# Kernel optimization log

Measured on AMD Instinct MI355X. Metric: run time of the kernel, lower is better.

## Reference

```python
import jax, jax.numpy as jnp
import numpy as np

B, H, W, C = 2, 64, 64, 96
DIN, NST, RNK, K = 192, 16, 6, 4
L = H * W


def _make_ids():
    idx = np.arange(L).reshape(H, W)
    p0 = idx.reshape(-1)
    p1 = idx.T.reshape(-1)
    p2 = p0[::-1].copy()
    p3 = p1[::-1].copy()
    scan = np.stack([p0, p1, p2, p3]).astype(np.int32)
    inv = np.stack([np.argsort(p) for p in scan]).astype(np.int32)
    return jnp.asarray(scan), jnp.asarray(inv)


def setup_inputs() -> dict:
    key = jax.random.key(0)
    ks = jax.random.split(key, 10)
    scan_ids, inv_ids = _make_ids()
    std = RNK ** -0.5
    # dt bias init: inverse-softplus of dt ~ LogUniform(1e-3, 1e-1), as in VMM.dt_init
    u = jax.random.uniform(ks[5], (K, DIN))
    dt = jnp.exp(u * (np.log(0.1) - np.log(0.001)) + np.log(0.001))
    dt_b = dt + jnp.log(-jnp.expm1(-dt))
    return {
        "x": jax.random.normal(ks[0], (B, H, W, C), jnp.float32),
        "W_in": jax.random.normal(ks[1], (2 * DIN, C), jnp.float32) * 0.02,
        "conv_w": jax.random.normal(ks[2], (DIN, 1, 3, 3), jnp.float32) * 0.1,
        "conv_b": jnp.zeros((DIN,), jnp.float32),
        "x_proj_w": jax.random.normal(ks[3], (K, RNK + 2 * NST, DIN), jnp.float32) * 0.02,
        "dt_w": jax.random.uniform(ks[4], (K, DIN, RNK), jnp.float32, -std, std),
        "dt_b": dt_b.astype(jnp.float32),
        "A_logs": jnp.log(jnp.tile(jnp.arange(1, NST + 1, dtype=jnp.float32)[None], (K * DIN, 1))),
        "Ds": jnp.ones((K * DIN,), jnp.float32),
        "gate_w": jax.random.normal(ks[6], (4 * DIN, 4), jnp.float32) * 0.1,  # grouped 1x1 conv, groups=DIN
        "gate_b": jnp.zeros((4 * DIN,), jnp.float32),
        "ln_g": jnp.ones((DIN,), jnp.float32),
        "ln_b": jnp.zeros((DIN,), jnp.float32),
        "W_out": jax.random.normal(ks[7], (C, DIN), jnp.float32) * 0.02,
        "scan_ids": scan_ids,
        "inv_ids": inv_ids,
    }


def _forward(x, W_in, conv_w, conv_b, x_proj_w, dt_w, dt_b, A_logs, Ds, gate_w, gate_b, ln_g, ln_b, W_out, scan_ids, inv_ids):
    b, h, w, c = x.shape
    l = h * w
    din = conv_w.shape[0]
    k = x_proj_w.shape[0]
    nst = A_logs.shape[1]
    rnk = dt_w.shape[2]
    # in_proj + split into x / gate z
    xz = x @ W_in.T
    xc, z = jnp.split(xz, 2, axis=-1)
    xc = jnp.transpose(xc, (0, 3, 1, 2))  # (b, din, h, w)
    # depthwise 3x3 conv + SiLU
    xc = jax.lax.conv_general_dilated(
        xc, conv_w, (1, 1), "SAME", feature_group_count=din,
        dimension_numbers=("NCHW", "OIHW", "NCHW")) + conv_b[None, :, None, None]
    xc = jax.nn.silu(xc)
    # multi-directional gather (mair_ids_scan)
    xf = xc.reshape(b, din, l)
    xs = jnp.moveaxis(xf[:, :, scan_ids], 2, 1)  # (b, k, din, l)
    # x_proj (grouped 1x1 conv) -> dt, B, C
    x_dbl = jnp.einsum("bkdl,krd->bkrl", xs, x_proj_w)
    dts, Bs, Cs = jnp.split(x_dbl, [rnk, rnk + nst], axis=2)  # (b,k,rnk,l),(b,k,n,l),(b,k,n,l)
    delta = jax.nn.softplus(jnp.einsum("bkrl,kdr->bkdl", dts, dt_w) + dt_b[None, :, :, None])
    A = -jnp.exp(A_logs).reshape(k, din, nst)
    dA = jnp.exp(delta[..., None] * A[None, :, :, None, :])              # (b,k,d,l,n)
    dBu = (delta * xs)[..., None] * jnp.moveaxis(Bs, 2, 3)[:, :, None]   # (b,k,d,l,n)

    def step(hst, inp):
        da, dbu = inp
        hst = da * hst + dbu
        return hst, hst

    h0 = jnp.zeros((b, k, din, nst), jnp.float32)
    _, hs = jax.lax.scan(step, h0, (jnp.moveaxis(dA, 3, 0), jnp.moveaxis(dBu, 3, 0)))  # (l,b,k,d,n)
    ys = jnp.einsum("lbkdn,bknl->bkdl", hs, Cs) + xs * Ds.reshape(k, din)[None, :, :, None]
    # inverse scatter (mair_ids_inverse) + concat along channels
    y = jax.vmap(lambda yk, ik: yk[..., ik], in_axes=(1, 0), out_axes=1)(ys, inv_ids)
    y = y.reshape(b, k * din, h, w)
    # ShuffleAttn gating: group = din, group_channels = k
    shuf = y.reshape(b, k, din, h, w).transpose(0, 2, 1, 3, 4).reshape(b, k * din, h, w)
    pooled = shuf.mean(axis=(2, 3)).reshape(b, din, k)
    gate = jax.nn.sigmoid(jnp.einsum("bgi,goi->bgo", pooled, gate_w.reshape(din, k, k)) + gate_b.reshape(din, k))
    gate = gate.transpose(0, 2, 1).reshape(b, k * din)  # channel_rearrange
    y = y * gate[:, :, None, None]
    # sum the 4 direction branches
    y = y.reshape(b, k, din, h, w).sum(axis=1)
    y = jnp.transpose(y, (0, 2, 3, 1))  # (b,h,w,din)
    # LayerNorm(d_inner)
    mu = y.mean(-1, keepdims=True)
    var = ((y - mu) ** 2).mean(-1, keepdims=True)
    y = (y - mu) / jnp.sqrt(var + 1e-5) * ln_g + ln_b
    y = y * jax.nn.silu(z)
    return y @ W_out.T


def reference(x, W_in, conv_w, conv_b, x_proj_w, dt_w, dt_b, A_logs, Ds, gate_w, gate_b, ln_g, ln_b, W_out, scan_ids, inv_ids):
    return _forward(x, W_in, conv_w, conv_b, x_proj_w, dt_w, dt_b, A_logs, Ds, gate_w, gate_b, ln_g, ln_b, W_out, scan_ids, inv_ids)
```

## Files before the change

kernel.cpp:

```cpp
#include <hip/hip_runtime.h>
#include <math.h>

#define BB 2
#define CC 96
#define DIN 192
#define NST 16
#define RNK 6
#define KK 4
#define LL 4096
#define RTOT (RNK + 2*NST)


__global__ __launch_bounds__(256) void k_inproj(const float* __restrict__ x,
        const float* __restrict__ W_in, float* __restrict__ xc_pre,
        float* __restrict__ z_silu) {
    __shared__ float lx[96*65];
    __shared__ float wt[48*196];
    int b = blockIdx.y, z = blockIdx.z;
    int l0 = blockIdx.x * 64;
    int t = threadIdx.x;
    for (int i = 0; i < 24; ++i) {
        int e = t + 256*i;
        int l = e / 96, c = e % 96;
        lx[c*65 + l] = x[((size_t)(b*LL + l0 + l))*96 + c];
    }
    int lg = t & 15;
    int og = t >> 4;
    float acc[4][12];
    #pragma unroll
    for (int j = 0; j < 4; ++j)
        #pragma unroll
        for (int q = 0; q < 12; ++q) acc[j][q] = 0.f;
    for (int p = 0; p < 2; ++p) {
        __syncthreads();
        for (int i = 0; i < 36; ++i) {
            int e = t + 256*i;
            int cc = e % 48, oc = e / 48;
            wt[cc*196 + oc] = W_in[((size_t)(z*192 + oc))*96 + p*48 + cc];
        }
        __syncthreads();
        #pragma unroll 2
        for (int cc = 0; cc < 48; ++cc) {
            int c = p*48 + cc;
            float x0 = lx[c*65 + 4*lg + 0];
            float x1 = lx[c*65 + 4*lg + 1];
            float x2 = lx[c*65 + 4*lg + 2];
            float x3 = lx[c*65 + 4*lg + 3];
            const float* wr = &wt[cc*196 + 12*og];
            float4 w0 = *(const float4*)(wr);
            float4 w1 = *(const float4*)(wr + 4);
            float4 w2 = *(const float4*)(wr + 8);
            float wv[12] = {w0.x,w0.y,w0.z,w0.w, w1.x,w1.y,w1.z,w1.w,
                            w2.x,w2.y,w2.z,w2.w};
            #pragma unroll
            for (int q = 0; q < 12; ++q) {
                acc[0][q] += x0*wv[q];
                acc[1][q] += x1*wv[q];
                acc[2][q] += x2*wv[q];
                acc[3][q] += x3*wv[q];
            }
        }
    }
    float* dst = (z == 0) ? xc_pre : z_silu;
    #pragma unroll
    for (int j = 0; j < 4; ++j) {
        int l = l0 + 4*lg + j;
        size_t base = (size_t)(b*LL + l)*DIN + 12*og;
        #pragma unroll
        for (int q = 0; q < 12; ++q) {
            float v = acc[j][q];
            if (z) v = v / (1.f + __expf(-v));
            dst[base + q] = v;
        }
    }
}

__global__ __launch_bounds__(256) void k_conv(const float* __restrict__ xc,
        const float* __restrict__ cw, const float* __restrict__ cb,
        float* __restrict__ out) {
    int gid = blockIdx.x*256 + threadIdx.x;
    int d = gid % DIN;
    int r = gid / DIN;
    int l = r & 4095, b = r >> 12;
    int w = l & 63, h = l >> 6;
    float acc = cb[d];
    #pragma unroll
    for (int dh = -1; dh <= 1; ++dh) {
        int h2 = h + dh;
        bool okh = (h2 >= 0) && (h2 < 64);
        #pragma unroll
        for (int dw = -1; dw <= 1; ++dw) {
            int w2 = w + dw;
            if (okh && w2 >= 0 && w2 < 64)
                acc += xc[((size_t)(b*LL + h2*64 + w2))*DIN + d] * cw[d*9 + (dh+1)*3 + (dw+1)];
        }
    }
    out[((size_t)(b*LL + l))*DIN + d] = acc / (1.f + __expf(-acc));
}

__global__ __launch_bounds__(512) void k_proj(const float* __restrict__ xconv,
        const int* __restrict__ scan_ids, const float* __restrict__ xpw,
        float* __restrict__ dts, float* __restrict__ Bs, float* __restrict__ Cs) {
    __shared__ float lxs[96*65];
    __shared__ float lw[RTOT*96];
    __shared__ float lbc[64*33];
    __shared__ int lsid[64];
    int k = blockIdx.y, b = blockIdx.z;
    int l0 = blockIdx.x * 64;
    int t = threadIdx.x;
    if (t < 64) lsid[t] = scan_ids[k*LL + l0 + t];
    int l = t & 63;
    int rg = __builtin_amdgcn_readfirstlane(t >> 6);
    float acc[5];
    #pragma unroll
    for (int j = 0; j < 5; ++j) acc[j] = 0.f;
    for (int p = 0; p < 2; ++p) {
        __syncthreads();
        for (int i = 0; i < 12; ++i) {
            int e = t + 512*i;
            int dd = e % 96, ll = e / 96;
            lxs[dd*65 + ll] = xconv[((size_t)(b*LL + lsid[ll]))*DIN + p*96 + dd];
        }
        for (int i = 0; i < 8; ++i) {
            int e = t + 512*i;
            if (e < RTOT*96) {
                int r = e / 96, dd = e % 96;
                lw[r*96 + dd] = xpw[(size_t)k*RTOT*DIN + r*DIN + p*96 + dd];
            }
        }
        __syncthreads();
        for (int dd = 0; dd < 96; dd += 4) {
            float x0 = lxs[(dd+0)*65 + l];
            float x1 = lxs[(dd+1)*65 + l];
            float x2 = lxs[(dd+2)*65 + l];
            float x3 = lxs[(dd+3)*65 + l];
            #pragma unroll
            for (int j = 0; j < 5; ++j) {
                int r = rg + 8*j;
                if (r < RTOT) {
                    float4 w = *(const float4*)&lw[r*96 + dd];
                    acc[j] += x0*w.x + x1*w.y + x2*w.z + x3*w.w;
                }
            }
        }
    }
    int bk = b*KK + k;
    #pragma unroll
    for (int j = 0; j < 5; ++j) {
        int r = rg + 8*j;
        if (r < RNK)       dts[((size_t)bk*LL + l0 + l)*8 + r] = acc[j];
        else if (r < RTOT) lbc[l*33 + (r - RNK)] = acc[j];
    }
    __syncthreads();
    size_t rowb = ((size_t)bk*LL + l0)*NST;
    for (int i = 0; i < 2; ++i) {
        int e = t + 512*i;
        int n = e & 15, ll = e >> 4;
        Bs[rowb + ll*NST + n] = lbc[ll*33 + n];
        Cs[rowb + ll*NST + n] = lbc[ll*33 + 16 + n];
    }
}

__global__ __launch_bounds__(384) void k_scan1(const float* __restrict__ xconv,
        const float* __restrict__ Bs, const float* __restrict__ Cs,
        const float* __restrict__ dts, const float* __restrict__ dtw,
        const float* __restrict__ dtb,
        const int* __restrict__ scan_ids, const float* __restrict__ A_logs,
        const float* __restrict__ Ds,
        float* __restrict__ y_dirs, float* __restrict__ segA,
        float* __restrict__ segB, int SL) {
    int seg = blockIdx.x, bk = blockIdx.y;
    int b = bk >> 2, k = bk & 3;
    int t = threadIdx.x;
    int half = t & 1, d = t >> 1;
    int l0 = seg * SL;
    float Av[8];
    {
        const float4* ap = (const float4*)(A_logs + ((k*DIN + d)*NST + half*8));
        float4 a0 = ap[0], a1 = ap[1];
        Av[0]=-__expf(a0.x); Av[1]=-__expf(a0.y); Av[2]=-__expf(a0.z); Av[3]=-__expf(a0.w);
        Av[4]=-__expf(a1.x); Av[5]=-__expf(a1.y); Av[6]=-__expf(a1.z); Av[7]=-__expf(a1.w);
    }
    float Dv = Ds[k*DIN + d];
    float wdt[RNK];
    float bdt = dtb[k*DIN + d];
    #pragma unroll
    for (int r = 0; r < RNK; ++r) wdt[r] = dtw[(k*DIN + d)*RNK + r];
    float h[8];
    #pragma unroll
    for (int n = 0; n < 8; ++n) h[n] = 0.f;
    float sumdv = 0.f;
    const int* sid = scan_ids + k*LL + l0;
    int ln = sid[0];
    float xn = xconv[((size_t)(b*LL + ln))*DIN + d];
    for (int li = 0; li < SL; ++li) {
        int l = ln;
        float xv = xn;
        if (li + 1 < SL) {
            ln = sid[li + 1];
            xn = xconv[((size_t)(b*LL + ln))*DIN + d];
        }
        const float* dr = dts + ((size_t)bk*LL + l0 + li)*8;
        float aa = bdt;
        #pragma unroll
        for (int r = 0; r < RNK; ++r) aa += dr[r]*wdt[r];
        float dv = fmaxf(aa, 0.f) + __logf(1.f + __expf(-fabsf(aa)));
        sumdv += dv;
        float dxv = dv * xv;
        const float* br = Bs + ((size_t)bk*LL + l0 + li)*NST + half*8;
        const float* cr = Cs + ((size_t)bk*LL + l0 + li)*NST + half*8;
        float4 b0 = *(const float4*)br;
        float4 b1 = *(const float4*)(br + 4);
        float4 c0v = *(const float4*)cr;
        float4 c1v = *(const float4*)(cr + 4);
        float bb[8] = {b0.x,b0.y,b0.z,b0.w, b1.x,b1.y,b1.z,b1.w};
        float cc[8] = {c0v.x,c0v.y,c0v.z,c0v.w, c1v.x,c1v.y,c1v.z,c1v.w};
        float y = 0.f;
        #pragma unroll
        for (int n = 0; n < 8; ++n) {
            float e2 = __expf(dv * Av[n]);
            h[n] = e2*h[n] + dxv*bb[n];
            y += h[n]*cc[n];
        }
        y += __shfl_xor(y, 1);
        if (half == 0) {
            y += xv * Dv;
            y_dirs[((size_t)(bk*LL + l))*DIN + d] = y;
        }
    }
    float a[8];
    #pragma unroll
    for (int n = 0; n < 8; ++n) a[n] = __expf(Av[n]*sumdv);
    size_t base = (((size_t)bk*gridDim.x + seg)*DIN + d)*NST + half*8;
    *(float4*)&segA[base]     = make_float4(a[0],a[1],a[2],a[3]);
    *(float4*)&segA[base + 4] = make_float4(a[4],a[5],a[6],a[7]);
    *(float4*)&segB[base]     = make_float4(h[0],h[1],h[2],h[3]);
    *(float4*)&segB[base + 4] = make_float4(h[4],h[5],h[6],h[7]);
}

__global__ __launch_bounds__(256) void k_scan2(const float* segA,
        const float* segB, float* hinit, int SEGC) {
    int idx = blockIdx.x*256 + threadIdx.x;
    if (idx >= BB*KK*DIN*NST) return;
    int bk = idx / (DIN*NST);
    int dn = idx % (DIN*NST);
    const size_t stride = DIN*NST;
    size_t o = (size_t)bk*SEGC*stride + dn;
    float h = 0.f;
    for (int s = 0; s < SEGC; s += 8) {
        float av[8], bv[8];
        #pragma unroll
        for (int j = 0; j < 8; ++j) {
            av[j] = segA[o + j*stride];
            bv[j] = segB[o + j*stride];
        }
        #pragma unroll
        for (int j = 0; j < 8; ++j) {
            hinit[o + j*stride] = h;
            h = av[j]*h + bv[j];
        }
        o += 8*stride;
    }
}

__global__ __launch_bounds__(384) void k_apply(const float* __restrict__ Cs,
        const float* __restrict__ dts, const float* __restrict__ dtw,
        const float* __restrict__ dtb,
        const int* __restrict__ scan_ids, const float* __restrict__ A_logs,
        const float* __restrict__ hinit,
        float* __restrict__ y_dirs, float* __restrict__ poolsum, int SL) {
    int seg = blockIdx.x, bk = blockIdx.y;
    int b = bk >> 2, k = bk & 3;
    int t = threadIdx.x;
    int half = t & 1, d = t >> 1;
    int l0 = seg * SL;
    float Av[8];
    {
        const float4* ap = (const float4*)(A_logs + ((k*DIN + d)*NST + half*8));
        float4 a0 = ap[0], a1 = ap[1];
        Av[0]=-__expf(a0.x); Av[1]=-__expf(a0.y); Av[2]=-__expf(a0.z); Av[3]=-__expf(a0.w);
        Av[4]=-__expf(a1.x); Av[5]=-__expf(a1.y); Av[6]=-__expf(a1.z); Av[7]=-__expf(a1.w);
    }
    float Av0 = -__expf(A_logs[(k*DIN + d)*NST]);
    bool okl = true;
    #pragma unroll
    for (int q = 0; q < 8; ++q) {
        float m = (float)(half*8 + q + 1);
        okl = okl && (fabsf(Av[q] - m*Av0) <= 1e-4f*m);
    }
    int fast = __all(okl);
    float h0[8];
    {
        size_t base = (((size_t)bk*gridDim.x + seg)*DIN + d)*NST + half*8;
        float4 v0 = *(const float4*)&hinit[base];
        float4 v1 = *(const float4*)&hinit[base + 4];
        h0[0]=v0.x; h0[1]=v0.y; h0[2]=v0.z; h0[3]=v0.w;
        h0[4]=v1.x; h0[5]=v1.y; h0[6]=v1.z; h0[7]=v1.w;
    }
    float wdt[RNK];
    float bdt = dtb[k*DIN + d];
    #pragma unroll
    for (int r = 0; r < RNK; ++r) wdt[r] = dtw[(k*DIN + d)*RNK + r];
    float cum = 0.f;
    float pool = 0.f;
    const int* sid = scan_ids + k*LL + l0;
    for (int li = 0; li < SL; ++li) {
        int l = sid[li];
        const float* dr = dts + ((size_t)bk*LL + l0 + li)*8;
        float aa = bdt;
        #pragma unroll
        for (int r = 0; r < RNK; ++r) aa += dr[r]*wdt[r];
        cum += fmaxf(aa, 0.f) + __logf(1.f + __expf(-fabsf(aa)));
        const float* cr = Cs + ((size_t)bk*LL + l0 + li)*NST + half*8;
        float4 c0v = *(const float4*)cr;
        float4 c1v = *(const float4*)(cr + 4);
        float cc[8] = {c0v.x,c0v.y,c0v.z,c0v.w, c1v.x,c1v.y,c1v.z,c1v.w};
        float g;
        if (fast) {
            float E = __expf(Av0 * cum);
            g = 0.f;
            #pragma unroll
            for (int q = 7; q >= 0; --q) g = g*E + cc[q]*h0[q];
            g *= E;
            if (half) {
                float E2 = E*E, E4 = E2*E2;
                g *= E4*E4;
            }
        } else {
            g = 0.f;
            #pragma unroll
            for (int q = 0; q < 8; ++q)
                g += cc[q]*h0[q]*__expf(Av[q]*cum);
        }
        g += __shfl_xor(g, 1);
        if (half == 0) {
            size_t yo = ((size_t)(bk*LL + l))*DIN + d;
            float y = y_dirs[yo] + g;
            y_dirs[yo] = y;
            pool += y;
        }
    }
    if (half == 0) atomicAdd(&poolsum[(b*DIN + d)*KK + k], pool);
}

__global__ __launch_bounds__(256) void k_final(const float* __restrict__ y_dirs,
        const float* __restrict__ poolsum, const float* __restrict__ gw,
        const float* __restrict__ gb, const float* __restrict__ z_silu,
        const float* __restrict__ lng, const float* __restrict__ lnb,
        const float* __restrict__ Wout, float* __restrict__ out) {
    __shared__ float buf[16*193];
    __shared__ float lgate[DIN*KK];
    __shared__ float lmu[16], lrs[16];
    int b = blockIdx.y;
    int l0 = blockIdx.x * 16;
    int t = threadIdx.x;
    for (int e = t; e < DIN*KK; e += 256) {
        int d = e >> 2, o = e & 3;
        float acc = gb[d*KK + o];
        #pragma unroll
        for (int i = 0; i < KK; ++i)
            acc += (poolsum[(b*DIN + d)*KK + i] * (1.f/LL)) * gw[(d*KK + o)*KK + i];
        lgate[d*KK + o] = 1.f/(1.f + __expf(-acc));
    }
    __syncthreads();
    for (int i = 0; i < 12; ++i) {
        int e = t + 256*i;
        int d = e % DIN, l = e / DIN;
        float acc = 0.f;
        #pragma unroll
        for (int k = 0; k < KK; ++k)
            acc += y_dirs[((size_t)((b*KK + k)*LL + l0 + l))*DIN + d] * lgate[d*KK + k];
        buf[l*193 + d] = acc;
    }
    __syncthreads();
    int l2 = t >> 4, q = t & 15;
    float s = 0.f, s2 = 0.f;
    for (int i = 0; i < 12; ++i) {
        float v = buf[l2*193 + q + 16*i];
        s += v; s2 += v*v;
    }
    s += __shfl_xor(s, 1);  s2 += __shfl_xor(s2, 1);
    s += __shfl_xor(s, 2);  s2 += __shfl_xor(s2, 2);
    s += __shfl_xor(s, 4);  s2 += __shfl_xor(s2, 4);
    s += __shfl_xor(s, 8);  s2 += __shfl_xor(s2, 8);
    if (q == 0) {
        float mu = s * (1.f/DIN);
        float var = s2 * (1.f/DIN) - mu*mu;
        lmu[l2] = mu;
        lrs[l2] = rsqrtf(var + 1e-5f);
    }
    __syncthreads();
    for (int i = 0; i < 12; ++i) {
        int e = t + 256*i;
        int d = e % DIN, l = e / DIN;
        float v = buf[l*193 + d];
        float tv = (v - lmu[l]) * lrs[l] * lng[d] + lnb[d];
        tv *= z_silu[((size_t)(b*LL + l0 + l))*DIN + d];
        buf[l*193 + d] = tv;
    }
    __syncthreads();
    int l = t & 15;
    int c0 = (t >> 4) * 6;
    float acc[6];
    #pragma unroll
    for (int cc = 0; cc < 6; ++cc) acc[cc] = 0.f;
    for (int d = 0; d < DIN; ++d) {
        float v = buf[l*193 + d];
        #pragma unroll
        for (int cc = 0; cc < 6; ++cc)
            acc[cc] += v * Wout[(c0 + cc)*DIN + d];
    }
    #pragma unroll
    for (int cc = 0; cc < 6; ++cc)
        out[((size_t)(b*LL + l0 + l))*CC + c0 + cc] = acc[cc];
}

extern "C" void kernel_launch(void* const* d_in, const int* in_sizes, int n_in,
                              void* d_out, int out_size, void* d_ws, size_t ws_size,
                              hipStream_t stream) {
    const float* x      = (const float*)d_in[0];
    const float* W_in   = (const float*)d_in[1];
    const float* conv_w = (const float*)d_in[2];
    const float* conv_b = (const float*)d_in[3];
    const float* xpw    = (const float*)d_in[4];
    const float* dt_w   = (const float*)d_in[5];
    const float* dt_b   = (const float*)d_in[6];
    const float* A_logs = (const float*)d_in[7];
    const float* Ds     = (const float*)d_in[8];
    const float* gate_w = (const float*)d_in[9];
    const float* gate_b = (const float*)d_in[10];
    const float* ln_g   = (const float*)d_in[11];
    const float* ln_b   = (const float*)d_in[12];
    const float* W_out  = (const float*)d_in[13];
    const int* scan_ids = (const int*)d_in[14];
    float* out = (float*)d_out;

    const size_t baseF = 6291456ull + 2ull*1572864 + 262144ull + 2ull*524288 + 3072;
    int SEGC = 16;
    if ((baseF + 2ull*128*24576)*4 <= ws_size) SEGC = 128;
    else if ((baseF + 2ull*64*24576)*4 <= ws_size) SEGC = 64;
    else if ((baseF + 2ull*32*24576)*4 <= ws_size) SEGC = 32;
    int SL = LL / SEGC;
    size_t segF = (size_t)SEGC * 24576;

    float* ws      = (float*)d_ws;
    float* y_dirs  = ws;
    float* xc_pre  = ws;
    float* z_silu  = y_dirs  + 6291456;
    float* xconv   = z_silu  + 1572864;
    float* dts     = xconv   + 1572864;
    float* Bs      = dts     + 262144;
    float* Cs      = Bs      + 524288;
    float* poolsum = Cs      + 524288;
    float* segA    = poolsum + 3072;
    float* segB    = segA    + segF;
    float* hinit   = segA;

    hipMemsetAsync(poolsum, 0, 1536*sizeof(float), stream);

    k_inproj<<<dim3(LL/64, BB, 2), 256, 0, stream>>>(x, W_in, xc_pre, z_silu);
    k_conv<<<(BB*DIN*LL)/256, 256, 0, stream>>>(xc_pre, conv_w, conv_b, xconv);
    k_proj<<<dim3(LL/64, KK, BB), 512, 0, stream>>>(xconv, scan_ids, xpw,
                                                    dts, Bs, Cs);
    k_scan1<<<dim3(SEGC, BB*KK), 384, 0, stream>>>(xconv, Bs, Cs, dts, dt_w, dt_b,
                                                   scan_ids, A_logs, Ds,
                                                   y_dirs, segA, segB, SL);
    k_scan2<<<(BB*KK*DIN*NST + 255)/256, 256, 0, stream>>>(segA, segB, hinit, SEGC);
    k_apply<<<dim3(SEGC, BB*KK), 384, 0, stream>>>(Cs, dts, dt_w, dt_b,
                                                   scan_ids, A_logs, hinit,
                                                   y_dirs, poolsum, SL);
    k_final<<<dim3(LL/16, BB), 256, 0, stream>>>(y_dirs, poolsum, gate_w, gate_b,
                                                 z_silu, ln_g, ln_b, W_out, out);
}
```

Before: 280.4 us.

## Vectorize global loads and stores with float4 and prefetch scan operands

Several kernels switch to float4 global loads and stores: the in-projection staging and output, the depthwise conv (each thread now handles 4 channels with weights in registers), the gathers in the x-projection, and the gating, LayerNorm and out-projection stages of the final kernel. The in-projection now loops over both halves (x and gate) inside one block, so the input tile is loaded once, at the price of half as many blocks. The scan and apply loops software-prefetch the next step's dt, B and C values into registers to hide load latency on the serial recurrence. The final buffer's row stride is padded to 196 so rows stay 16-byte aligned for float4 access.

```diff
diff --git a/kernel.cpp b/kernel.cpp
--- a/kernel.cpp
+++ b/kernel.cpp
@@ -16,61 +16,74 @@
         float* __restrict__ z_silu) {
     __shared__ float lx[96*65];
     __shared__ float wt[48*196];
-    int b = blockIdx.y, z = blockIdx.z;
+    int b = blockIdx.y;
     int l0 = blockIdx.x * 64;
     int t = threadIdx.x;
-    for (int i = 0; i < 24; ++i) {
-        int e = t + 256*i;
-        int l = e / 96, c = e % 96;
-        lx[c*65 + l] = x[((size_t)(b*LL + l0 + l))*96 + c];
+    for (int i = 0; i < 6; ++i) {
+        int e4 = t + 256*i;
+        int c4 = e4 % 24, l = e4 / 24;
+        float4 v = *(const float4*)&x[((size_t)(b*LL + l0 + l))*96 + 4*c4];
+        lx[(4*c4+0)*65 + l] = v.x;
+        lx[(4*c4+1)*65 + l] = v.y;
+        lx[(4*c4+2)*65 + l] = v.z;
+        lx[(4*c4+3)*65 + l] = v.w;
     }
     int lg = t & 15;
     int og = t >> 4;
-    float acc[4][12];
-    #pragma unroll
-    for (int j = 0; j < 4; ++j)
-        #pragma unroll
-        for (int q = 0; q < 12; ++q) acc[j][q] = 0.f;
-    for (int p = 0; p < 2; ++p) {
-        __syncthreads();
-        for (int i = 0; i < 36; ++i) {
-            int e = t + 256*i;
-            int cc = e % 48, oc = e / 48;
-            wt[cc*196 + oc] = W_in[((size_t)(z*192 + oc))*96 + p*48 + cc];
-        }
-        __syncthreads();
-        #pragma unroll 2
-        for (int cc = 0; cc < 48; ++cc) {
-            int c = p*48 + cc;
-            float x0 = lx[c*65 + 4*lg + 0];
-            float x1 = lx[c*65 + 4*lg + 1];
-            float x2 = lx[c*65 + 4*lg + 2];
-            float x3 = lx[c*65 + 4*lg + 3];
-            const float* wr = &wt[cc*196 + 12*og];
-            float4 w0 = *(const float4*)(wr);
-            float4 w1 = *(const float4*)(wr + 4);
-            float4 w2 = *(const float4*)(wr + 8);
-            float wv[12] = {w0.x,w0.y,w0.z,w0.w, w1.x,w1.y,w1.z,w1.w,
-                            w2.x,w2.y,w2.z,w2.w};
+    for (int z = 0; z < 2; ++z) {
+        float acc[4][12];
+        #pragma unroll
+        for (int j = 0; j < 4; ++j)
+            #pragma unroll
+            for (int q = 0; q < 12; ++q) acc[j][q] = 0.f;
+        for (int p = 0; p < 2; ++p) {
+            __syncthreads();
+            for (int i = 0; i < 9; ++i) {
+                int e4 = t + 256*i;
+                int cc4 = e4 % 12, oc = e4 / 12;
+                float4 v = *(const float4*)&W_in[((size_t)(z*192 + oc))*96 + p*48 + 4*cc4];
+                wt[(4*cc4+0)*196 + oc] = v.x;
+                wt[(4*cc4+1)*196 + oc] = v.y;
+                wt[(4*cc4+2)*196 + oc] = v.z;
+                wt[(4*cc4+3)*196 + oc] = v.w;
+            }
+            __syncthreads();
+            #pragma unroll 2
+            for (int cc = 0; cc < 48; ++cc) {
+                int c = p*48 + cc;
+                float x0 = lx[c*65 + 4*lg + 0];
+                float x1 = lx[c*65 + 4*lg + 1];
+                float x2 = lx[c*65 + 4*lg + 2];
+                float x3 = lx[c*65 + 4*lg + 3];
+                const float* wr = &wt[cc*196 + 12*og];
+                float4 w0 = *(const float4*)(wr);
+                float4 w1 = *(const float4*)(wr + 4);
+                float4 w2 = *(const float4*)(wr + 8);
+                float wv[12] = {w0.x,w0.y,w0.z,w0.w, w1.x,w1.y,w1.z,w1.w,
+                                w2.x,w2.y,w2.z,w2.w};
+                #pragma unroll
+                for (int q = 0; q < 12; ++q) {
+                    acc[0][q] += x0*wv[q];
+                    acc[1][q] += x1*wv[q];
+                    acc[2][q] += x2*wv[q];
+                    acc[3][q] += x3*wv[q];
+                }
+            }
+        }
+        float* dst = (z == 0) ? xc_pre : z_silu;
+        #pragma unroll
+        for (int j = 0; j < 4; ++j) {
+            int l = l0 + 4*lg + j;
+            size_t base = (size_t)(b*LL + l)*DIN + 12*og;
+            float v[12];
             #pragma unroll
             for (int q = 0; q < 12; ++q) {
-                acc[0][q] += x0*wv[q];
-                acc[1][q] += x1*wv[q];
-                acc[2][q] += x2*wv[q];
-                acc[3][q] += x3*wv[q];
-            }
-        }
-    }
-    float* dst = (z == 0) ? xc_pre : z_silu;
-    #pragma unroll
-    for (int j = 0; j < 4; ++j) {
-        int l = l0 + 4*lg + j;
-        size_t base = (size_t)(b*LL + l)*DIN + 12*og;
-        #pragma unroll
-        for (int q = 0; q < 12; ++q) {
-            float v = acc[j][q];
-            if (z) v = v / (1.f + __expf(-v));
-            dst[base + q] = v;
+                float a = acc[j][q];
+                v[q] = z ? a/(1.f + __expf(-a)) : a;
+            }
+            *(float4*)&dst[base]     = make_float4(v[0],v[1],v[2],v[3]);
+            *(float4*)&dst[base + 4] = make_float4(v[4],v[5],v[6],v[7]);
+            *(float4*)&dst[base + 8] = make_float4(v[8],v[9],v[10],v[11]);
         }
     }
 }
@@ -79,11 +92,17 @@
         const float* __restrict__ cw, const float* __restrict__ cb,
         float* __restrict__ out) {
     int gid = blockIdx.x*256 + threadIdx.x;
-    int d = gid % DIN;
-    int r = gid / DIN;
+    int dq = gid % 48;
+    int r = gid / 48;
     int l = r & 4095, b = r >> 12;
     int w = l & 63, h = l >> 6;
-    float acc = cb[d];
+    int d0 = dq*4;
+    float4 acc = *(const float4*)&cb[d0];
+    float wreg[4][9];
+    #pragma unroll
+    for (int j = 0; j < 4; ++j)
+        #pragma unroll
+        for (int tp = 0; tp < 9; ++tp) wreg[j][tp] = cw[(d0+j)*9 + tp];
     #pragma unroll
     for (int dh = -1; dh <= 1; ++dh) {
         int h2 = h + dh;
@@ -91,11 +110,22 @@
         #pragma unroll
         for (int dw = -1; dw <= 1; ++dw) {
             int w2 = w + dw;
-            if (okh && w2 >= 0 && w2 < 64)
-                acc += xc[((size_t)(b*LL + h2*64 + w2))*DIN + d] * cw[d*9 + (dh+1)*3 + (dw+1)];
-        }
-    }
-    out[((size_t)(b*LL + l))*DIN + d] = acc / (1.f + __expf(-acc));
+            if (okh && w2 >= 0 && w2 < 64) {
+                float4 v = *(const float4*)&xc[((size_t)(b*LL + h2*64 + w2))*DIN + d0];
+                int tp = (dh+1)*3 + (dw+1);
+                acc.x += v.x*wreg[0][tp];
+                acc.y += v.y*wreg[1][tp];
+                acc.z += v.z*wreg[2][tp];
+                acc.w += v.w*wreg[3][tp];
+            }
+        }
+    }
+    float4 o;
+    o.x = acc.x/(1.f + __expf(-acc.x));
+    o.y = acc.y/(1.f + __expf(-acc.y));
+    o.z = acc.z/(1.f + __expf(-acc.z));
+    o.w = acc.w/(1.f + __expf(-acc.w));
+    *(float4*)&out[((size_t)(b*LL + l))*DIN + d0] = o;
 }
 
 __global__ __launch_bounds__(512) void k_proj(const float* __restrict__ xconv,
@@ -116,16 +146,21 @@
     for (int j = 0; j < 5; ++j) acc[j] = 0.f;
     for (int p = 0; p < 2; ++p) {
         __syncthreads();
-        for (int i = 0; i < 12; ++i) {
-            int e = t + 512*i;
-            int dd = e % 96, ll = e / 96;
-            lxs[dd*65 + ll] = xconv[((size_t)(b*LL + lsid[ll]))*DIN + p*96 + dd];
-        }
-        for (int i = 0; i < 8; ++i) {
-            int e = t + 512*i;
-            if (e < RTOT*96) {
-                int r = e / 96, dd = e % 96;
-                lw[r*96 + dd] = xpw[(size_t)k*RTOT*DIN + r*DIN + p*96 + dd];
+        for (int i = 0; i < 3; ++i) {
+            int e4 = t + 512*i;
+            int dd4 = e4 % 24, ll = e4 / 24;
+            float4 v = *(const float4*)&xconv[((size_t)(b*LL + lsid[ll]))*DIN + p*96 + 4*dd4];
+            lxs[(4*dd4+0)*65 + ll] = v.x;
+            lxs[(4*dd4+1)*65 + ll] = v.y;
+            lxs[(4*dd4+2)*65 + ll] = v.z;
+            lxs[(4*dd4+3)*65 + ll] = v.w;
+        }
+        for (int i = 0; i < 2; ++i) {
+            int e4 = t + 512*i;
+            if (e4 < RTOT*24) {
+                int r = e4 / 24, dd4 = e4 % 24;
+                *(float4*)&lw[r*96 + 4*dd4] =
+                    *(const float4*)&xpw[(size_t)k*RTOT*DIN + r*DIN + p*96 + 4*dd4];
             }
         }
         __syncthreads();
@@ -191,28 +226,39 @@
     for (int n = 0; n < 8; ++n) h[n] = 0.f;
     float sumdv = 0.f;
     const int* sid = scan_ids + k*LL + l0;
+    const float* dbase = dts + ((size_t)bk*LL + l0)*8;
+    const float* bbase = Bs + ((size_t)bk*LL + l0)*NST + half*8;
+    const float* cbase = Cs + ((size_t)bk*LL + l0)*NST + half*8;
     int ln = sid[0];
     float xn = xconv[((size_t)(b*LL + ln))*DIN + d];
+    float drc[RNK];
+    #pragma unroll
+    for (int r = 0; r < RNK; ++r) drc[r] = dbase[r];
+    float4 bn0 = *(const float4*)bbase,      bn1 = *(const float4*)(bbase + 4);
+    float4 cn0 = *(const float4*)cbase,      cn1 = *(const float4*)(cbase + 4);
     for (int li = 0; li < SL; ++li) {
         int l = ln;
         float xv = xn;
+        float drv[RNK];
+        #pragma unroll
+        for (int r = 0; r < RNK; ++r) drv[r] = drc[r];
+        float4 b0 = bn0, b1 = bn1, c0v = cn0, c1v = cn1;
         if (li + 1 < SL) {
             ln = sid[li + 1];
             xn = xconv[((size_t)(b*LL + ln))*DIN + d];
-        }
-        const float* dr = dts + ((size_t)bk*LL + l0 + li)*8;
+            #pragma unroll
+            for (int r = 0; r < RNK; ++r) drc[r] = dbase[(li+1)*8 + r];
+            bn0 = *(const float4*)(bbase + (size_t)(li+1)*NST);
+            bn1 = *(const float4*)(bbase + (size_t)(li+1)*NST + 4);
+            cn0 = *(const float4*)(cbase + (size_t)(li+1)*NST);
+            cn1 = *(const float4*)(cbase + (size_t)(li+1)*NST + 4);
+        }
         float aa = bdt;
         #pragma unroll
-        for (int r = 0; r < RNK; ++r) aa += dr[r]*wdt[r];
+        for (int r = 0; r < RNK; ++r) aa += drv[r]*wdt[r];
         float dv = fmaxf(aa, 0.f) + __logf(1.f + __expf(-fabsf(aa)));
         sumdv += dv;
         float dxv = dv * xv;
-        const float* br = Bs + ((size_t)bk*LL + l0 + li)*NST + half*8;
-        const float* cr = Cs + ((size_t)bk*LL + l0 + li)*NST + half*8;
-        float4 b0 = *(const float4*)br;
-        float4 b1 = *(const float4*)(br + 4);
-        float4 c0v = *(const float4*)cr;
-        float4 c1v = *(const float4*)(cr + 4);
         float bb[8] = {b0.x,b0.y,b0.z,b0.w, b1.x,b1.y,b1.z,b1.w};
         float cc[8] = {c0v.x,c0v.y,c0v.z,c0v.w, c1v.x,c1v.y,c1v.z,c1v.w};
         float y = 0.f;
@@ -304,16 +350,28 @@
     float cum = 0.f;
     float pool = 0.f;
     const int* sid = scan_ids + k*LL + l0;
+    const float* dbase = dts + ((size_t)bk*LL + l0)*8;
+    const float* cbase = Cs + ((size_t)bk*LL + l0)*NST + half*8;
+    float drc[RNK];
+    #pragma unroll
+    for (int r = 0; r < RNK; ++r) drc[r] = dbase[r];
+    float4 cn0 = *(const float4*)cbase, cn1 = *(const float4*)(cbase + 4);
     for (int li = 0; li < SL; ++li) {
         int l = sid[li];
-        const float* dr = dts + ((size_t)bk*LL + l0 + li)*8;
+        float drv[RNK];
+        #pragma unroll
+        for (int r = 0; r < RNK; ++r) drv[r] = drc[r];
+        float4 c0v = cn0, c1v = cn1;
+        if (li + 1 < SL) {
+            #pragma unroll
+            for (int r = 0; r < RNK; ++r) drc[r] = dbase[(li+1)*8 + r];
+            cn0 = *(const float4*)(cbase + (size_t)(li+1)*NST);
+            cn1 = *(const float4*)(cbase + (size_t)(li+1)*NST + 4);
+        }
         float aa = bdt;
         #pragma unroll
-        for (int r = 0; r < RNK; ++r) aa += dr[r]*wdt[r];
+        for (int r = 0; r < RNK; ++r) aa += drv[r]*wdt[r];
         cum += fmaxf(aa, 0.f) + __logf(1.f + __expf(-fabsf(aa)));
-        const float* cr = Cs + ((size_t)bk*LL + l0 + li)*NST + half*8;
-        float4 c0v = *(const float4*)cr;
-        float4 c1v = *(const float4*)(cr + 4);
         float cc[8] = {c0v.x,c0v.y,c0v.z,c0v.w, c1v.x,c1v.y,c1v.z,c1v.w};
         float g;
         if (fast) {
@@ -348,7 +406,7 @@
         const float* __restrict__ gb, const float* __restrict__ z_silu,
         const float* __restrict__ lng, const float* __restrict__ lnb,
         const float* __restrict__ Wout, float* __restrict__ out) {
-    __shared__ float buf[16*193];
+    __shared__ float buf[16*196];
     __shared__ float lgate[DIN*KK];
     __shared__ float lmu[16], lrs[16];
     int b = blockIdx.y;
@@ -363,20 +421,26 @@
         lgate[d*KK + o] = 1.f/(1.f + __expf(-acc));
     }
     __syncthreads();
-    for (int i = 0; i < 12; ++i) {
-        int e = t + 256*i;
-        int d = e % DIN, l = e / DIN;
-        float acc = 0.f;
-        #pragma unroll
-        for (int k = 0; k < KK; ++k)
-            acc += y_dirs[((size_t)((b*KK + k)*LL + l0 + l))*DIN + d] * lgate[d*KK + k];
-        buf[l*193 + d] = acc;
+    for (int i = 0; i < 3; ++i) {
+        int e4 = t + 256*i;
+        int d4 = e4 % 48, l = e4 / 48;
+        int db = 4*d4;
+        float4 acc = make_float4(0.f, 0.f, 0.f, 0.f);
+        #pragma unroll
+        for (int k = 0; k < KK; ++k) {
+            float4 v = *(const float4*)&y_dirs[((size_t)((b*KK + k)*LL + l0 + l))*DIN + db];
+            acc.x += v.x * lgate[(db+0)*KK + k];
+            acc.y += v.y * lgate[(db+1)*KK + k];
+            acc.z += v.z * lgate[(db+2)*KK + k];
+            acc.w += v.w * lgate[(db+3)*KK + k];
+        }
+        *(float4*)&buf[l*196 + db] = acc;
     }
     __syncthreads();
     int l2 = t >> 4, q = t & 15;
     float s = 0.f, s2 = 0.f;
     for (int i = 0; i < 12; ++i) {
-        float v = buf[l2*193 + q + 16*i];
+        float v = buf[l2*196 + q + 16*i];
         s += v; s2 += v*v;
     }
     s += __shfl_xor(s, 1);  s2 += __shfl_xor(s2, 1);
@@ -390,13 +454,20 @@
         lrs[l2] = rsqrtf(var + 1e-5f);
     }
     __syncthreads();
-    for (int i = 0; i < 12; ++i) {
-        int e = t + 256*i;
-        int d = e % DIN, l = e / DIN;
-        float v = buf[l*193 + d];
-        float tv = (v - lmu[l]) * lrs[l] * lng[d] + lnb[d];
-        tv *= z_silu[((size_t)(b*LL + l0 + l))*DIN + d];
-        buf[l*193 + d] = tv;
+    for (int i = 0; i < 3; ++i) {
+        int e4 = t + 256*i;
+        int d4 = e4 % 48, l = e4 / 48;
+        int db = 4*d4;
+        float4 v  = *(float4*)&buf[l*196 + db];
+        float4 g4 = *(const float4*)&lng[db];
+        float4 b4 = *(const float4*)&lnb[db];
+        float4 z4 = *(const float4*)&z_silu[((size_t)(b*LL + l0 + l))*DIN + db];
+        float mu = lmu[l], rs = lrs[l];
+        v.x = ((v.x - mu)*rs*g4.x + b4.x) * z4.x;
+        v.y = ((v.y - mu)*rs*g4.y + b4.y) * z4.y;
+        v.z = ((v.z - mu)*rs*g4.z + b4.z) * z4.z;
+        v.w = ((v.w - mu)*rs*g4.w + b4.w) * z4.w;
+        *(float4*)&buf[l*196 + db] = v;
     }
     __syncthreads();
     int l = t & 15;
@@ -404,11 +475,13 @@
     float acc[6];
     #pragma unroll
     for (int cc = 0; cc < 6; ++cc) acc[cc] = 0.f;
-    for (int d = 0; d < DIN; ++d) {
-        float v = buf[l*193 + d];
-        #pragma unroll
-        for (int cc = 0; cc < 6; ++cc)
-            acc[cc] += v * Wout[(c0 + cc)*DIN + d];
+    for (int d4 = 0; d4 < 48; ++d4) {
+        float4 v = *(float4*)&buf[l*196 + 4*d4];
+        #pragma unroll
+        for (int cc = 0; cc < 6; ++cc) {
+            float4 w = *(const float4*)&Wout[(c0 + cc)*DIN + 4*d4];
+            acc[cc] += v.x*w.x + v.y*w.y + v.z*w.z + v.w*w.w;
+        }
     }
     #pragma unroll
     for (int cc = 0; cc < 6; ++cc)
@@ -458,8 +531,8 @@
 
     hipMemsetAsync(poolsum, 0, 1536*sizeof(float), stream);
 
-    k_inproj<<<dim3(LL/64, BB, 2), 256, 0, stream>>>(x, W_in, xc_pre, z_silu);
-    k_conv<<<(BB*DIN*LL)/256, 256, 0, stream>>>(xc_pre, conv_w, conv_b, xconv);
+    k_inproj<<<dim3(LL/64, BB), 256, 0, stream>>>(x, W_in, xc_pre, z_silu);
+    k_conv<<<(BB*LL*48)/256, 256, 0, stream>>>(xc_pre, conv_w, conv_b, xconv);
     k_proj<<<dim3(LL/64, KK, BB), 512, 0, stream>>>(xconv, scan_ids, xpw,
                                                     dts, Bs, Cs);
     k_scan1<<<dim3(SEGC, BB*KK), 384, 0, stream>>>(xconv, Bs, Cs, dts, dt_w, dt_b,
```

Result: slower. 286.7 us (+2.2%).
